# Optimization experiments

Hardware: AMD Instinct MI355X
Metric: run time of the kernel (lower is better)

## Reference

```python
import jax, jax.numpy as jnp
import numpy as np

MU = 0.75
H = W = 256


def _bending_energy_one(pred):
    """pred: (2, 256, 256) probabilities. Returns scalar bending energy."""
    mask = (pred[1] > 0.5).astype(jnp.float32)  # (H, W) binary nucleus mask
    p = jnp.pad(mask, 1)
    # 8-neighbor count (3x3 ones kernel with zero center)
    nc = (p[:-2, :-2] + p[:-2, 1:-1] + p[:-2, 2:] +
          p[1:-1, :-2] + p[1:-1, 2:] +
          p[2:, :-2] + p[2:, 1:-1] + p[2:, 2:])
    contour = (mask == 1.0) & (nc < 8.0)  # (H, W) bool
    flat = contour.reshape(-1)            # (H*W,)
    N = flat.shape[0]
    # Stable argsort puts contour pixel indices first, in ascending
    # (row-major) order == torch.nonzero ordering. Fixed output shape.
    order = jnp.argsort(~flat, stable=True)  # (N,) int
    m = flat.sum()                            # number of contour points
    rows = (order // W).astype(jnp.float32)
    cols = (order % W).astype(jnp.float32)
    pts = jnp.stack([rows, cols], axis=-1)    # (N, 2)

    v1 = pts[1:-1] - pts[:-2]   # point - prev_point, centers 1..N-2
    v2 = pts[2:] - pts[1:-1]    # next_point - point
    cross = v1[:, 0] * v2[:, 1] - v1[:, 1] * v2[:, 0]
    dot = (v1 * v2).sum(-1)
    n1 = jnp.sqrt((v1 ** 2).sum(-1))
    n2 = jnp.sqrt((v2 ** 2).sum(-1))
    curv = jnp.where(cross == 0.0, 0.0,
                     2.0 * jnp.abs(cross) / (n1 * n2 + dot))
    delta = jnp.where(cross >= 0.0, 0.0, 1.0)
    be = (1.0 - delta + delta * MU) * curv ** 2 / (n1 + n2)
    # valid centers are indices 1..m-2 of the contour list -> j <= m-3
    j = jnp.arange(N - 2)
    valid = j <= (m - 3)
    return jnp.where(valid, be, 0.0).sum()


def setup_inputs() -> dict:
    key = jax.random.key(0)
    k1, k2 = jax.random.split(key)
    B = 128
    inp = jax.random.normal(k1, (B, 2, H, W), dtype=jnp.float32)
    tgt = jax.random.uniform(k2, (B, 2, H, W), dtype=jnp.float32)
    return {"input": inp, "target": tgt}


def reference(input, target):
    per_image = jax.vmap(_bending_energy_one)(target)  # (B,)
    return per_image.sum() / input.shape[0]
```

## Files before the change

kernel.cpp:

```cpp
#include <hip/hip_runtime.h>

typedef unsigned long long ull;
#define NW 1024

__global__ __launch_bounds__(512)
void ballot_kernel(const float* __restrict__ target,
                   ull* __restrict__ mbg,
                   float* __restrict__ out) {
    const int lane = threadIdx.x & 63;
    const int gw = blockIdx.x * 8 + (threadIdx.x >> 6);

    if (gw == 0 && lane == 0) out[0] = 0.0f;

    #pragma unroll 4
    for (int i = 0; i < 16; ++i) {
        const int w = gw + i * 8192;
        const int img = w >> 10, k = w & 1023;
        float v = target[(size_t)img * 131072 + 65536 + (k << 6) + lane];
        ull b = __ballot(v > 0.5f);
        if (lane == 0) mbg[w] = b;
    }
}

__global__ __launch_bounds__(1024)
void energy_kernel(const ull* __restrict__ mbg,
                   float* __restrict__ out, float inv_b) {
#pragma clang fp contract(off)
    __shared__ ull mask[NW];
    __shared__ unsigned short idx[65536];
    __shared__ int   wsums[16];
    __shared__ float fsum[16];

    const int img  = blockIdx.x;
    const int tid  = threadIdx.x;
    const int wave = tid >> 6, lane = tid & 63;

    mask[tid] = mbg[(size_t)img * NW + tid];
    __syncthreads();

    ull w;
    {
        const int r = tid >> 2, wp = tid & 3;
        auto get = [&](int rr, int ww) -> ull {
            return (rr < 0 || rr > 255 || ww < 0 || ww > 3)
                       ? 0ULL : mask[(rr << 2) + ww];
        };
        ull A  = get(r - 1, wp);
        ull C  = mask[tid];
        ull Bx = get(r + 1, wp);
        ull Ap = get(r - 1, wp - 1), An = get(r - 1, wp + 1);
        ull Cp = get(r,     wp - 1), Cn = get(r,     wp + 1);
        ull Bp = get(r + 1, wp - 1), Bn = get(r + 1, wp + 1);
        ull interior =
            ((A  << 1) | (Ap >> 63)) & A  & ((A  >> 1) | (An << 63)) &
            ((C  << 1) | (Cp >> 63)) &      ((C  >> 1) | (Cn << 63)) &
            ((Bx << 1) | (Bp >> 63)) & Bx & ((Bx >> 1) | (Bn << 63));
        w = C & ~interior;
    }

    const int pc = __popcll(w);
    int c = pc;
    for (int d = 1; d < 64; d <<= 1) {
        int t = __shfl_up(c, d);
        if (lane >= d) c += t;
    }
    if (lane == 63) wsums[wave] = c;
    __syncthreads();
    if (wave == 0 && lane < 16) {
        int s = wsums[lane];
        for (int d = 1; d < 16; d <<= 1) {
            int t = __shfl_up(s, d, 16);
            if (lane >= d) s += t;
        }
        wsums[lane] = s;
    }
    __syncthreads();

    int pos = c - pc + (wave > 0 ? wsums[wave - 1] : 0);
    const int base = tid << 6;
    while (w) {
        int b = __builtin_ctzll(w);
        w &= w - 1;
        idx[pos++] = (unsigned short)(base + b);
    }
    const int m = wsums[15];
    __syncthreads();

    float sum = 0.0f;
    for (int j = tid; j < m - 2; j += 1024) {
        const int p0 = idx[j], p1 = idx[j + 1], p2 = idx[j + 2];
        float r0f = (float)(p0 >> 8), c0f = (float)(p0 & 255);
        float r1f = (float)(p1 >> 8), c1f = (float)(p1 & 255);
        float r2f = (float)(p2 >> 8), c2f = (float)(p2 & 255);
        float v1r = r1f - r0f, v1c = c1f - c0f;
        float v2r = r2f - r1f, v2c = c2f - c1f;
        float cross = v1r * v2c - v1c * v2r;
        if (cross != 0.0f) {
            float dot = v1r * v2r + v1c * v2c;
            float n1 = sqrtf(v1r * v1r + v1c * v1c);
            float n2 = sqrtf(v2r * v2r + v2c * v2c);
            float curv = (2.0f * fabsf(cross)) / (n1 * n2 + dot);
            float factor = (cross >= 0.0f) ? 1.0f : 0.75f;
            sum += (factor * (curv * curv)) / (n1 + n2);
        }
    }

    for (int off = 32; off > 0; off >>= 1) sum += __shfl_down(sum, off);
    if (lane == 0) fsum[wave] = sum;
    __syncthreads();
    if (tid == 0) {
        float t = 0.0f;
        for (int i = 0; i < 16; ++i) t += fsum[i];
        atomicAdd(out, t * inv_b);
    }
}

extern "C" void kernel_launch(void* const* d_in, const int* in_sizes, int n_in,
                              void* d_out, int out_size, void* d_ws, size_t ws_size,
                              hipStream_t stream) {
    const float* target = (const float*)d_in[1];
    float* out = (float*)d_out;
    const int B = in_sizes[1] / (2 * 256 * 256);
    ull* mbg = (ull*)d_ws;

    ballot_kernel<<<dim3(B * 8), dim3(512), 0, stream>>>(target, mbg, out);
    energy_kernel<<<dim3(B), dim3(1024), 0, stream>>>(mbg, out, 1.0f / (float)B);
}
```

Before: 148.3 us.

## Fuse ballot mask construction into energy kernel and split each image across two blocks

Removes the separate ballot kernel and its global mask buffer: each 1024-thread block now reads the channel-1 plane directly, builds the bitmask in shared memory with wave ballots, then does contour extraction and the energy sum. Each image is handled by two blocks that both rebuild the mask, prefix sum and index list, then split the energy loop between them. This aims to remove a launch and the global round trip, and to fill all CUs with twice as many blocks. The cost is duplicated mask and scan work and doubled reads of the target data. The atomic add is skipped when a block's partial sum is zero. The old zeroing of the output is gone, so correctness now relies on the harness clearing the output beforehand.

```diff
diff --git a/kernel.cpp b/kernel.cpp
--- a/kernel.cpp
+++ b/kernel.cpp
@@ -3,39 +3,32 @@
 typedef unsigned long long ull;
 #define NW 1024
 
-__global__ __launch_bounds__(512)
-void ballot_kernel(const float* __restrict__ target,
-                   ull* __restrict__ mbg,
-                   float* __restrict__ out) {
-    const int lane = threadIdx.x & 63;
-    const int gw = blockIdx.x * 8 + (threadIdx.x >> 6);
-
-    if (gw == 0 && lane == 0) out[0] = 0.0f;
-
-    #pragma unroll 4
-    for (int i = 0; i < 16; ++i) {
-        const int w = gw + i * 8192;
-        const int img = w >> 10, k = w & 1023;
-        float v = target[(size_t)img * 131072 + 65536 + (k << 6) + lane];
-        ull b = __ballot(v > 0.5f);
-        if (lane == 0) mbg[w] = b;
-    }
-}
-
 __global__ __launch_bounds__(1024)
-void energy_kernel(const ull* __restrict__ mbg,
-                   float* __restrict__ out, float inv_b) {
+void bending_fused_kernel(const float* __restrict__ target,
+                          float* __restrict__ out, float inv_b) {
 #pragma clang fp contract(off)
     __shared__ ull mask[NW];
     __shared__ unsigned short idx[65536];
     __shared__ int   wsums[16];
     __shared__ float fsum[16];
 
-    const int img  = blockIdx.x;
+    const int img  = blockIdx.x >> 1;
+    const int half = blockIdx.x & 1;
     const int tid  = threadIdx.x;
     const int wave = tid >> 6, lane = tid & 63;
 
-    mask[tid] = mbg[(size_t)img * NW + tid];
+    const float* imgp = target + (size_t)img * 131072 + 65536;
+
+    {
+        const int k0 = wave << 6;
+        #pragma unroll 8
+        for (int i = 0; i < 64; ++i) {
+            const int k = k0 + i;
+            float v = imgp[(k << 6) + lane];
+            ull b = __ballot(v > 0.5f);
+            if (lane == 0) mask[k] = b;
+        }
+    }
     __syncthreads();
 
     ull w;
@@ -87,7 +80,7 @@
     __syncthreads();
 
     float sum = 0.0f;
-    for (int j = tid; j < m - 2; j += 1024) {
+    for (int j = (half << 10) + tid; j < m - 2; j += 2048) {
         const int p0 = idx[j], p1 = idx[j + 1], p2 = idx[j + 2];
         float r0f = (float)(p0 >> 8), c0f = (float)(p0 & 255);
         float r1f = (float)(p1 >> 8), c1f = (float)(p1 & 255);
@@ -111,7 +104,7 @@
     if (tid == 0) {
         float t = 0.0f;
         for (int i = 0; i < 16; ++i) t += fsum[i];
-        atomicAdd(out, t * inv_b);
+        if (t != 0.0f) atomicAdd(out, t * inv_b);
     }
 }
 
@@ -121,8 +114,7 @@
     const float* target = (const float*)d_in[1];
     float* out = (float*)d_out;
     const int B = in_sizes[1] / (2 * 256 * 256);
-    ull* mbg = (ull*)d_ws;
 
-    ballot_kernel<<<dim3(B * 8), dim3(512), 0, stream>>>(target, mbg, out);
-    energy_kernel<<<dim3(B), dim3(1024), 0, stream>>>(mbg, out, 1.0f / (float)B);
+    bending_fused_kernel<<<dim3(B * 2), dim3(1024), 0, stream>>>(
+        target, out, 1.0f / (float)B);
 }
```

Measured after the change: 146.6 us. No clear change (-1.2%).
